# Kernel tuning notes

Measured on AMD Instinct MI355X. Metric: run time of the kernel, lower is better.

Reference implementation:

```python
import jax, jax.numpy as jnp
import numpy as np

HEADS = 16

def _binarize(W):
    # alpha: per-output-row mean of |W| (reduce over all dims except dim 0)
    alpha = jnp.mean(jnp.abs(W), axis=tuple(range(1, W.ndim)), keepdims=True)
    # straight-through sign: forward sign(W), backward identity
    B = W + jax.lax.stop_gradient(jnp.sign(W) - W)
    return alpha * B

def _binlinear(x, W, b):
    Wb = _binarize(W)
    return jnp.einsum('btc,oc->bto', x, Wb) + b

def setup_inputs() -> dict:
    key = jax.random.key(0)
    ks = jax.random.split(key, 9)
    dim = 1024
    B, T = 4, 2048
    inp = {
        'x': jax.random.normal(ks[0], (B, T, dim), jnp.float32),
        'Wq': jax.random.normal(ks[1], (dim, dim), jnp.float32) * 0.02,
        'bq': jax.random.normal(ks[2], (dim,), jnp.float32) * 0.02,
        'Wk': jax.random.normal(ks[3], (dim, dim), jnp.float32) * 0.02,
        'bk': jax.random.normal(ks[4], (dim,), jnp.float32) * 0.02,
        'Wv': jax.random.normal(ks[5], (dim, dim), jnp.float32) * 0.02,
        'bv': jax.random.normal(ks[6], (dim,), jnp.float32) * 0.02,
        'Wp': jax.random.normal(ks[7], (dim, dim), jnp.float32) * 0.02,
        'bp': jax.random.normal(ks[8], (dim,), jnp.float32) * 0.02,
    }
    return inp

def reference(x, Wq, bq, Wk, bk, Wv, bv, Wp, bp):
    B, T, C = x.shape
    H = HEADS
    Dh = C // H
    scale = Dh ** -0.5

    def split_heads(t):
        return t.reshape(B, T, H, Dh).transpose(0, 2, 1, 3)  # [B,H,T,Dh]

    q = split_heads(_binlinear(x, Wq, bq))
    k = split_heads(_binlinear(x, Wk, bk))
    v = split_heads(_binlinear(x, Wv, bv))

    att = jnp.einsum('bhtd,bhsd->bhts', q, k) * scale  # [B,H,T,T]
    att = jax.nn.softmax(att, axis=-1)
    y = jnp.einsum('bhts,bhsd->bhtd', att, v)  # [B,H,T,Dh]
    y = y.transpose(0, 2, 1, 3).reshape(B, T, C)
    return _binlinear(y, Wp, bp)
```

## Files before the change

kernel.cpp:

```cpp
#include <hip/hip_runtime.h>
#include <hip/hip_bf16.h>

typedef short s16x8 __attribute__((ext_vector_type(8)));
typedef float f32x4 __attribute__((ext_vector_type(4)));
typedef unsigned u32x4 __attribute__((ext_vector_type(4)));
typedef unsigned short u16;

#define LOG2E 1.4426950408889634f
#define QSC (0.125f * LOG2E)

typedef __attribute__((address_space(3))) unsigned int lds_u32;
typedef __attribute__((address_space(1))) const unsigned int glb_u32;

static __device__ __forceinline__ void gload16(const void* g, void* l) {
  __builtin_amdgcn_global_load_lds((glb_u32*)g, (lds_u32*)l, 16, 0, 0);
}
static __device__ __forceinline__ u16 bf16u(float f) {
  unsigned u = __builtin_bit_cast(unsigned, f);
  return (u16)((u + 0x7FFFu + ((u >> 16) & 1u)) >> 16);
}
static __device__ __forceinline__ unsigned pk(u16 a, u16 b) {
  return (unsigned)a | ((unsigned)b << 16);
}
static __device__ __forceinline__ unsigned cvtpk(float lo, float hi) {
  unsigned d;
  asm("v_cvt_pk_bf16_f32 %0, %1, %2" : "=v"(d) : "v"(lo), "v"(hi));
  return d;
}
static __device__ __forceinline__ unsigned pk2(float a, float b) {
  float2 f; f.x = a; f.y = b;
  __hip_bfloat162 h = __float22bfloat162_rn(f);
  unsigned r;
  __builtin_memcpy(&r, &h, 4);
  return r;
}

__global__ __launch_bounds__(256) void k_prep(
    const float* __restrict__ x, u16* __restrict__ xb,
    const float* __restrict__ Wq, const float* __restrict__ Wk,
    const float* __restrict__ Wv, const float* __restrict__ Wp,
    const float* __restrict__ bq, const float* __restrict__ bk,
    const float* __restrict__ bv, const float* __restrict__ bp,
    u16* __restrict__ wbqkv, u16* __restrict__ wbp,
    float* __restrict__ alphaf, float* __restrict__ biasf) {
  if (blockIdx.x >= 1024) {
    int i = ((blockIdx.x - 1024) * 256 + threadIdx.x) * 8;
    float4 a = *reinterpret_cast<const float4*>(x + i);
    float4 b = *reinterpret_cast<const float4*>(x + i + 4);
    uint4 w = { pk2(a.x, a.y), pk2(a.z, a.w), pk2(b.x, b.y), pk2(b.z, b.w) };
    *reinterpret_cast<uint4*>(xb + i) = w;
    return;
  }
  int wave = threadIdx.x >> 6, lane = threadIdx.x & 63;
  int row = blockIdx.x * 4 + wave;
  const float* src; const float* bias; int r;
  if (row < 1024)      { src = Wq; bias = bq; r = row; }
  else if (row < 2048) { src = Wk; bias = bk; r = row - 1024; }
  else if (row < 3072) { src = Wv; bias = bv; r = row - 2048; }
  else                 { src = Wp; bias = bp; r = row - 3072; }
  const float4* s4 = reinterpret_cast<const float4*>(src + r * 1024);
  float4 v[4];
  float asum = 0.f;
#pragma unroll
  for (int i = 0; i < 4; ++i) {
    v[i] = s4[lane * 4 + i];
    asum += fabsf(v[i].x) + fabsf(v[i].y) + fabsf(v[i].z) + fabsf(v[i].w);
  }
#pragma unroll
  for (int m = 32; m >= 1; m >>= 1) asum += __shfl_xor(asum, m, 64);
  float alpha = asum * (1.0f / 1024.0f);

  u16 o[16];
#pragma unroll
  for (int i = 0; i < 4; ++i) {
    const float* f = reinterpret_cast<const float*>(&v[i]);
#pragma unroll
    for (int j = 0; j < 4; ++j) {
      float w = f[j];
      o[i * 4 + j] = (w > 0.f) ? (u16)0x3F80 : ((w < 0.f) ? (u16)0xBF80 : (u16)0);
    }
  }
  u16* dst = (row < 3072 ? wbqkv + row * 1024 : wbp + (row - 3072) * 1024) + lane * 16;
  uint4 w0 = { pk(o[0],o[1]), pk(o[2],o[3]), pk(o[4],o[5]), pk(o[6],o[7]) };
  uint4 w1 = { pk(o[8],o[9]), pk(o[10],o[11]), pk(o[12],o[13]), pk(o[14],o[15]) };
  reinterpret_cast<uint4*>(dst)[0] = w0;
  reinterpret_cast<uint4*>(dst)[1] = w1;
  if (lane == 0) {
    float sc = (row < 1024) ? QSC : 1.0f;
    alphaf[row] = alpha * sc;
    biasf[row]  = bias[r] * sc;
  }
}

template <int MODE, int NX, int NWG>
__global__ __launch_bounds__(256) void k_gemm(
    const u16* __restrict__ A, const u16* __restrict__ Bw,
    const float* __restrict__ alphaf, const float* __restrict__ biasf,
    u16* __restrict__ qbuf, u16* __restrict__ kbuf, u16* __restrict__ vtbuf,
    float* __restrict__ outf) {
  __shared__ alignas(128) char smem[33792];
  char* As = smem;
  char* Bs = smem + 16384;
  int tid = threadIdx.x;
  int wave = tid >> 6, l = tid & 63, g = l >> 4, ln = l & 15;
  int wm = (wave >> 1) * 64, wn = (wave & 1) * 64;
  int wg = (blockIdx.x & 7) * (NWG / 8) + (blockIdx.x >> 3);
  int m0 = (wg / NX) * 128, n0 = (wg % NX) * 128;

  f32x4 acc[4][4];
#pragma unroll
  for (int i = 0; i < 4; ++i)
#pragma unroll
    for (int j = 0; j < 4; ++j) acc[i][j] = f32x4{0.f, 0.f, 0.f, 0.f};

  const char* Ab = reinterpret_cast<const char*>(A) + m0 * 2048;
  const char* Bb = reinterpret_cast<const char*>(Bw) + n0 * 2048;

  int soff[4];
#pragma unroll
  for (int i = 0; i < 4; ++i) {
    int P = i * 4096 + tid * 16;
    int r = P >> 7;
    int kc = ((P >> 4) & 7) ^ (r & 7);
    soff[i] = r * 2048 + kc * 16;
  }

  for (int ks = 0; ks < 16; ++ks) {
    int kb0 = ks * 128;
#pragma unroll
    for (int i = 0; i < 4; ++i)
      gload16(Ab + soff[i] + kb0, As + i * 4096 + wave * 1024);
#pragma unroll
    for (int i = 0; i < 4; ++i)
      gload16(Bb + soff[i] + kb0, Bs + i * 4096 + wave * 1024);
    __syncthreads();
#pragma unroll
    for (int kk = 0; kk < 2; ++kk) {
      s16x8 af[4], bfr[4];
#pragma unroll
      for (int mf = 0; mf < 4; ++mf) {
        int r = wm + mf * 16 + ln;
        int kb = (kk * 64 + g * 16) ^ ((r & 7) << 4);
        af[mf] = *reinterpret_cast<const s16x8*>(As + r * 128 + kb);
      }
#pragma unroll
      for (int nf = 0; nf < 4; ++nf) {
        int r = wn + nf * 16 + ln;
        int kb = (kk * 64 + g * 16) ^ ((r & 7) << 4);
        bfr[nf] = *reinterpret_cast<const s16x8*>(Bs + r * 128 + kb);
      }
#pragma unroll
      for (int mf = 0; mf < 4; ++mf)
#pragma unroll
        for (int nf = 0; nf < 4; ++nf)
          acc[mf][nf] = __builtin_amdgcn_mfma_f32_16x16x32_bf16(af[mf], bfr[nf], acc[mf][nf], 0, 0, 0);
    }
    __syncthreads();
  }

  if (MODE == 0) {
    if (n0 < 2048) {
      u16* dst = (n0 < 1024) ? qbuf : kbuf;
#pragma unroll
      for (int nf = 0; nf < 4; ++nf) {
        int n = n0 + wn + nf * 16 + ln;
        float al = alphaf[n], bi = biasf[n];
        int nl = n & 1023;
        int h = nl >> 6, d = nl & 63;
#pragma unroll
        for (int mf = 0; mf < 4; ++mf)
#pragma unroll
          for (int rg = 0; rg < 4; ++rg) {
            int m = m0 + wm + mf * 16 + g * 4 + rg;
            int b = m >> 11, t = m & 2047;
            dst[(((b * 16 + h) * 2048 + t) << 6) + d] = bf16u(al * acc[mf][nf][rg] + bi);
          }
      }
    } else {
      u16* ldsT = reinterpret_cast<u16*>(smem);
#pragma unroll
      for (int nf = 0; nf < 4; ++nf) {
        int n = n0 + wn + nf * 16 + ln;
        float al = alphaf[n], bi = biasf[n];
        int nloc = wn + nf * 16 + ln;
#pragma unroll
        for (int mf = 0; mf < 4; ++mf)
#pragma unroll
          for (int rg = 0; rg < 4; ++rg) {
            int mloc = wm + mf * 16 + g * 4 + rg;
            ldsT[mloc * 132 + nloc] = bf16u(al * acc[mf][nf][rg] + bi);
          }
      }
      __syncthreads();
      int dl = tid >> 1;
      int sh = (tid & 1) * 64;
      int nv = n0 - 2048 + dl;
      int h = nv >> 6, d = nv & 63;
      int b = m0 >> 11;
      int s0 = (m0 & 2047) + sh;
      u16* vdst = vtbuf + (((b * 16 + h) * 64 + d) << 11) + s0;
#pragma unroll
      for (int c8 = 0; c8 < 8; ++c8) {
        u16 t0 = ldsT[(sh + c8 * 8 + 0) * 132 + dl], t1 = ldsT[(sh + c8 * 8 + 1) * 132 + dl];
        u16 t2 = ldsT[(sh + c8 * 8 + 2) * 132 + dl], t3 = ldsT[(sh + c8 * 8 + 3) * 132 + dl];
        u16 t4 = ldsT[(sh + c8 * 8 + 4) * 132 + dl], t5 = ldsT[(sh + c8 * 8 + 5) * 132 + dl];
        u16 t6 = ldsT[(sh + c8 * 8 + 6) * 132 + dl], t7 = ldsT[(sh + c8 * 8 + 7) * 132 + dl];
        uint4 w = { pk(t0, t1), pk(t2, t3), pk(t4, t5), pk(t6, t7) };
        *reinterpret_cast<uint4*>(vdst + c8 * 8) = w;
      }
    }
  } else {
#pragma unroll
    for (int nf = 0; nf < 4; ++nf) {
      int n = n0 + wn + nf * 16 + ln;
      float al = alphaf[3072 + n], bi = biasf[3072 + n];
#pragma unroll
      for (int mf = 0; mf < 4; ++mf)
#pragma unroll
        for (int rg = 0; rg < 4; ++rg) {
          int m = m0 + wm + mf * 16 + g * 4 + rg;
          outf[m * 1024 + n] = al * acc[mf][nf][rg] + bi;
        }
    }
  }
}

__global__ __launch_bounds__(512, 4) void k_attn(
    const u16* __restrict__ qb, const u16* __restrict__ kb,
    const u16* __restrict__ vtb, u16* __restrict__ yb) {
  __shared__ alignas(128) char smem[32768];
  int tid = threadIdx.x;
  int wave = tid >> 6, lane = tid & 63;
  int g = lane >> 4, ln = lane & 15;

  int wg = (blockIdx.x & 7) * 64 + (blockIdx.x >> 3);
  int bh = wg >> 3, qt = wg & 7;
  const char* Qg = reinterpret_cast<const char*>(qb) + bh * 262144;
  const char* Kg = reinterpret_cast<const char*>(kb) + bh * 262144;
  const char* Vg = reinterpret_cast<const char*>(vtb) + bh * 262144;

  int qrow = qt * 256 + wave * 32 + ln;
  const s16x8* Qr0 = reinterpret_cast<const s16x8*>(Qg + qrow * 128);
  const s16x8* Qr1 = reinterpret_cast<const s16x8*>(Qg + (qrow + 16) * 128);
  s16x8 qf[2][2];
  qf[0][0] = Qr0[g]; qf[0][1] = Qr0[g + 4];
  qf[1][0] = Qr1[g]; qf[1][1] = Qr1[g + 4];

  s16x8 ones;
#pragma unroll
  for (int i = 0; i < 8; ++i) ones[i] = (short)0x3F80;

  int r = tid >> 3, kc = tid & 7;
  int wr = (r & 3) | (((r >> 3) & 1) << 2);
  int swsrc = (kc ^ wr) * 16;
  int ksrc = r * 128 + swsrc;
  int vsrc = r * 4096 + swsrc;

  int swK = (ln & 7) << 4;
  int swV = ((ln & 3) | (((ln >> 3) & 1) << 2)) << 4;

  f32x4 oacc[2][4];
#pragma unroll
  for (int s = 0; s < 2; ++s)
#pragma unroll
    for (int i = 0; i < 4; ++i) oacc[s][i] = f32x4{0.f, 0.f, 0.f, 0.f};
  f32x4 lacc[2];
  lacc[0] = f32x4{0.f, 0.f, 0.f, 0.f};
  lacc[1] = f32x4{0.f, 0.f, 0.f, 0.f};

  gload16(Kg + ksrc, smem + wave * 1024);
  gload16(Vg + vsrc, smem + 8192 + wave * 1024);
  __syncthreads();

  for (int st = 0; st < 32; ++st) {
    int cb = st & 1;
    if (st < 31) {
      int sb = (st + 1) * 64;
      char* nb = smem + (cb ^ 1) * 16384;
      gload16(Kg + sb * 128 + ksrc, nb + wave * 1024);
      gload16(Vg + sb * 2 + vsrc, nb + 8192 + wave * 1024);
    }
    const char* Kb = smem + cb * 16384;
    const char* Vb = Kb + 8192;

    f32x4 sacc[2][4];
#pragma unroll
    for (int s = 0; s < 2; ++s)
#pragma unroll
      for (int t = 0; t < 4; ++t) sacc[s][t] = f32x4{0.f, 0.f, 0.f, 0.f};
    __builtin_amdgcn_s_setprio(1);
#pragma unroll
    for (int kt = 0; kt < 2; ++kt) {
      int off = (kt * 64 + g * 16) ^ swK;
#pragma unroll
      for (int t = 0; t < 4; ++t) {
        int rho = 32 * (t & 1) + 8 * (ln >> 2) + 4 * (t >> 1) + (ln & 3);
        s16x8 kf = *reinterpret_cast<const s16x8*>(Kb + rho * 128 + off);
        sacc[0][t] = __builtin_amdgcn_mfma_f32_16x16x32_bf16(kf, qf[0][kt], sacc[0][t], 0, 0, 0);
        sacc[1][t] = __builtin_amdgcn_mfma_f32_16x16x32_bf16(kf, qf[1][kt], sacc[1][t], 0, 0, 0);
      }
    }
    __builtin_amdgcn_s_setprio(0);

    s16x8 pf[2][2];
#pragma unroll
    for (int s = 0; s < 2; ++s) {
      float p[4][4];
#pragma unroll
      for (int t = 0; t < 4; ++t)
#pragma unroll
        for (int rg = 0; rg < 4; ++rg)
          p[t][rg] = __builtin_amdgcn_exp2f(sacc[s][t][rg]);
#pragma unroll
      for (int kt = 0; kt < 2; ++kt) {
        u32x4 tw;
        tw[0] = cvtpk(p[kt][0],     p[kt][1]);
        tw[1] = cvtpk(p[kt][2],     p[kt][3]);
        tw[2] = cvtpk(p[kt + 2][0], p[kt + 2][1]);
        tw[3] = cvtpk(p[kt + 2][2], p[kt + 2][3]);
        pf[s][kt] = __builtin_bit_cast(s16x8, tw);
      }
    }

#pragma unroll
    for (int s = 0; s < 2; ++s)
#pragma unroll
      for (int kt = 0; kt < 2; ++kt)
        lacc[s] = __builtin_amdgcn_mfma_f32_16x16x32_bf16(ones, pf[s][kt], lacc[s], 0, 0, 0);

    __builtin_amdgcn_s_setprio(1);
#pragma unroll
    for (int kt = 0; kt < 2; ++kt) {
      int off = (kt * 64 + g * 16) ^ swV;
#pragma unroll
      for (int dt = 0; dt < 4; ++dt) {
        s16x8 vf = *reinterpret_cast<const s16x8*>(Vb + (dt * 16 + ln) * 128 + off);
        oacc[0][dt] = __builtin_amdgcn_mfma_f32_16x16x32_bf16(vf, pf[0][kt], oacc[0][dt], 0, 0, 0);
        oacc[1][dt] = __builtin_amdgcn_mfma_f32_16x16x32_bf16(vf, pf[1][kt], oacc[1][dt], 0, 0, 0);
      }
    }
    __builtin_amdgcn_s_setprio(0);
    __syncthreads();
  }

  int b = bh >> 4, h = bh & 15;
#pragma unroll
  for (int s = 0; s < 2; ++s) {
    float linv = 1.0f / lacc[s][0];
    u16* yrow = yb + (b * 2048 + qrow + s * 16) * 1024 + h * 64;
#pragma unroll
    for (int dt = 0; dt < 4; ++dt) {
      uint2 w;
      w.x = cvtpk(oacc[s][dt][0] * linv, oacc[s][dt][1] * linv);
      w.y = cvtpk(oacc[s][dt][2] * linv, oacc[s][dt][3] * linv);
      *reinterpret_cast<uint2*>(yrow + dt * 16 + g * 4) = w;
    }
  }
}

extern "C" void kernel_launch(void* const* d_in, const int* in_sizes, int n_in,
                              void* d_out, int out_size, void* d_ws, size_t ws_size,
                              hipStream_t stream) {
  (void)in_sizes; (void)n_in; (void)out_size; (void)ws_size;
  const float* x  = (const float*)d_in[0];
  const float* Wq = (const float*)d_in[1];
  const float* bq = (const float*)d_in[2];
  const float* Wk = (const float*)d_in[3];
  const float* bk = (const float*)d_in[4];
  const float* Wv = (const float*)d_in[5];
  const float* bv = (const float*)d_in[6];
  const float* Wp = (const float*)d_in[7];
  const float* bp = (const float*)d_in[8];

  char* ws = (char*)d_ws;
  u16*   xb    = (u16*)(ws);
  u16*   wbqkv = (u16*)(ws + 16777216);
  u16*   wbp   = (u16*)(ws + 23068672);
  float* alphaf = (float*)(ws + 25165824);
  float* biasf  = (float*)(ws + 25182208);
  u16*   vtbuf = (u16*)(ws + 25198592);
  u16*   ybuf  = xb;
  u16*   qbuf  = (u16*)d_out;
  u16*   kbuf  = (u16*)d_out + 8388608;
  float* outf  = (float*)d_out;

  k_prep<<<5120, 256, 0, stream>>>(x, xb, Wq, Wk, Wv, Wp, bq, bk, bv, bp, wbqkv, wbp, alphaf, biasf);
  k_gemm<0, 24, 1536><<<1536, 256, 0, stream>>>(xb, wbqkv, alphaf, biasf, qbuf, kbuf, vtbuf, nullptr);
  k_attn<<<512, 512, 0, stream>>>(qbuf, kbuf, vtbuf, ybuf);
  k_gemm<1, 8, 512><<<512, 256, 0, stream>>>(ybuf, wbp, alphaf, biasf, nullptr, nullptr, nullptr, outf);
}
```

Measured before the change: 165.1 us.

## Triple-buffer GEMM K-loop with async global-to-LDS prefetch two stages ahead

Replaces the single-buffered 128-wide K step in the projection GEMM with a three-stage ring of 64-wide K tiles. Loads for stage kt+2 are issued before computing stage kt, and explicit vmcnt waits plus one barrier per step replace the two syncthreads. The XOR swizzle is dropped, so the 64-byte-row LDS layout may cause bank conflicts on fragment reads, and LDS use rises to 48KB, which can lower occupancy.

```diff
diff --git a/kernel.cpp b/kernel.cpp
--- a/kernel.cpp
+++ b/kernel.cpp
@@ -98,9 +98,7 @@
     const float* __restrict__ alphaf, const float* __restrict__ biasf,
     u16* __restrict__ qbuf, u16* __restrict__ kbuf, u16* __restrict__ vtbuf,
     float* __restrict__ outf) {
-  __shared__ alignas(128) char smem[33792];
-  char* As = smem;
-  char* Bs = smem + 16384;
+  __shared__ alignas(128) char smem[49152];
   int tid = threadIdx.x;
   int wave = tid >> 6, l = tid & 63, g = l >> 4, ln = l & 15;
   int wm = (wave >> 1) * 64, wn = (wave & 1) * 64;
@@ -116,46 +114,50 @@
   const char* Ab = reinterpret_cast<const char*>(A) + m0 * 2048;
   const char* Bb = reinterpret_cast<const char*>(Bw) + n0 * 2048;
 
-  int soff[4];
-#pragma unroll
-  for (int i = 0; i < 4; ++i) {
-    int P = i * 4096 + tid * 16;
-    int r = P >> 7;
-    int kc = ((P >> 4) & 7) ^ (r & 7);
-    soff[i] = r * 2048 + kc * 16;
-  }
-
-  for (int ks = 0; ks < 16; ++ks) {
-    int kb0 = ks * 128;
-#pragma unroll
-    for (int i = 0; i < 4; ++i)
-      gload16(Ab + soff[i] + kb0, As + i * 4096 + wave * 1024);
-#pragma unroll
-    for (int i = 0; i < 4; ++i)
-      gload16(Bb + soff[i] + kb0, Bs + i * 4096 + wave * 1024);
-    __syncthreads();
-#pragma unroll
-    for (int kk = 0; kk < 2; ++kk) {
-      s16x8 af[4], bfr[4];
-#pragma unroll
-      for (int mf = 0; mf < 4; ++mf) {
-        int r = wm + mf * 16 + ln;
-        int kb = (kk * 64 + g * 16) ^ ((r & 7) << 4);
-        af[mf] = *reinterpret_cast<const s16x8*>(As + r * 128 + kb);
-      }
-#pragma unroll
-      for (int nf = 0; nf < 4; ++nf) {
-        int r = wn + nf * 16 + ln;
-        int kb = (kk * 64 + g * 16) ^ ((r & 7) << 4);
-        bfr[nf] = *reinterpret_cast<const s16x8*>(Bs + r * 128 + kb);
-      }
-#pragma unroll
-      for (int mf = 0; mf < 4; ++mf)
-#pragma unroll
-        for (int nf = 0; nf < 4; ++nf)
-          acc[mf][nf] = __builtin_amdgcn_mfma_f32_16x16x32_bf16(af[mf], bfr[nf], acc[mf][nf], 0, 0, 0);
-    }
-    __syncthreads();
+  int srow0 = tid >> 2;
+  int scol = (tid & 3) * 16;
+
+#define STAGE_G(kt)                                                          \
+  {                                                                          \
+    char* buf_ = smem + ((kt) % 3) * 16384;                                  \
+    _Pragma("unroll")                                                        \
+    for (int i_ = 0; i_ < 2; ++i_) {                                         \
+      gload16(Ab + (srow0 + 64 * i_) * 2048 + (kt) * 64 + scol,              \
+              buf_ + i_ * 4096 + wave * 1024);                               \
+      gload16(Bb + (srow0 + 64 * i_) * 2048 + (kt) * 64 + scol,              \
+              buf_ + 8192 + i_ * 4096 + wave * 1024);                        \
+    }                                                                        \
+  }
+
+  STAGE_G(0);
+  STAGE_G(1);
+  asm volatile("s_waitcnt vmcnt(4)" ::: "memory");
+  __builtin_amdgcn_sched_barrier(0);
+  __builtin_amdgcn_s_barrier();
+
+  for (int kt = 0; kt < 32; ++kt) {
+    if (kt < 30) STAGE_G(kt + 2);
+    const char* As = smem + (kt % 3) * 16384;
+    const char* Bs = As + 8192;
+    s16x8 af[4], bfr[4];
+#pragma unroll
+    for (int mf = 0; mf < 4; ++mf)
+      af[mf] = *reinterpret_cast<const s16x8*>(As + (wm + mf * 16 + ln) * 64 + g * 16);
+#pragma unroll
+    for (int nf = 0; nf < 4; ++nf)
+      bfr[nf] = *reinterpret_cast<const s16x8*>(Bs + (wn + nf * 16 + ln) * 64 + g * 16);
+#pragma unroll
+    for (int mf = 0; mf < 4; ++mf)
+#pragma unroll
+      for (int nf = 0; nf < 4; ++nf)
+        acc[mf][nf] = __builtin_amdgcn_mfma_f32_16x16x32_bf16(af[mf], bfr[nf], acc[mf][nf], 0, 0, 0);
+    if (kt < 30) {
+      asm volatile("s_waitcnt vmcnt(4)" ::: "memory");
+    } else {
+      asm volatile("s_waitcnt vmcnt(0)" ::: "memory");
+    }
+    __builtin_amdgcn_sched_barrier(0);
+    __builtin_amdgcn_s_barrier();
   }
 
   if (MODE == 0) {
@@ -223,6 +225,7 @@
         }
     }
   }
+#undef STAGE_G
 }
 
 __global__ __launch_bounds__(512, 4) void k_attn(
```

Measured after the change: 162.8 us. No clear change (-1.4%).

## Double-buffer A tiles in LDS and stream B fragments from global into registers

Applied to the files above, without the earlier changes.

Restructures the GEMM main loop into a software pipeline. The next A tile is prefetched into an alternate LDS buffer with global_load_lds while the current one feeds the MFMAs. B fragments now go straight from global memory into registers, prefetched one k-step ahead, and LDS staging for B is dropped. The loop uses one barrier per iteration with explicit vmcnt/lgkmcnt waits instead of two __syncthreads, and the kernel now requests 4 waves per SIMD through launch bounds. The goal is to hide load latency behind compute. The costs are more global traffic for B, since waves sharing a column block each fetch it, and more register pressure.

```diff
diff --git a/kernel.cpp b/kernel.cpp
--- a/kernel.cpp
+++ b/kernel.cpp
@@ -93,14 +93,12 @@
 }
 
 template <int MODE, int NX, int NWG>
-__global__ __launch_bounds__(256) void k_gemm(
+__global__ __launch_bounds__(256, 4) void k_gemm(
     const u16* __restrict__ A, const u16* __restrict__ Bw,
     const float* __restrict__ alphaf, const float* __restrict__ biasf,
     u16* __restrict__ qbuf, u16* __restrict__ kbuf, u16* __restrict__ vtbuf,
     float* __restrict__ outf) {
   __shared__ alignas(128) char smem[33792];
-  char* As = smem;
-  char* Bs = smem + 16384;
   int tid = threadIdx.x;
   int wave = tid >> 6, l = tid & 63, g = l >> 4, ln = l & 15;
   int wm = (wave >> 1) * 64, wn = (wave & 1) * 64;
@@ -124,38 +122,72 @@
     int kc = ((P >> 4) & 7) ^ (r & 7);
     soff[i] = r * 2048 + kc * 16;
   }
-
-  for (int ks = 0; ks < 16; ++ks) {
-    int kb0 = ks * 128;
-#pragma unroll
-    for (int i = 0; i < 4; ++i)
-      gload16(Ab + soff[i] + kb0, As + i * 4096 + wave * 1024);
-#pragma unroll
-    for (int i = 0; i < 4; ++i)
-      gload16(Bb + soff[i] + kb0, Bs + i * 4096 + wave * 1024);
-    __syncthreads();
-#pragma unroll
-    for (int kk = 0; kk < 2; ++kk) {
-      s16x8 af[4], bfr[4];
-#pragma unroll
-      for (int mf = 0; mf < 4; ++mf) {
-        int r = wm + mf * 16 + ln;
-        int kb = (kk * 64 + g * 16) ^ ((r & 7) << 4);
-        af[mf] = *reinterpret_cast<const s16x8*>(As + r * 128 + kb);
-      }
-#pragma unroll
-      for (int nf = 0; nf < 4; ++nf) {
-        int r = wn + nf * 16 + ln;
-        int kb = (kk * 64 + g * 16) ^ ((r & 7) << 4);
-        bfr[nf] = *reinterpret_cast<const s16x8*>(Bs + r * 128 + kb);
-      }
-#pragma unroll
-      for (int mf = 0; mf < 4; ++mf)
-#pragma unroll
-        for (int nf = 0; nf < 4; ++nf)
-          acc[mf][nf] = __builtin_amdgcn_mfma_f32_16x16x32_bf16(af[mf], bfr[nf], acc[mf][nf], 0, 0, 0);
-    }
-    __syncthreads();
+  const char* Brow[4];
+#pragma unroll
+  for (int nf = 0; nf < 4; ++nf) Brow[nf] = Bb + (wn + nf * 16 + ln) * 2048;
+
+  s16x8 bfr[2][4];
+
+#define STAGE_A(kt)                                                          \
+  {                                                                          \
+    char* buf_ = smem + ((kt) & 1) * 16384;                                  \
+    _Pragma("unroll")                                                        \
+    for (int i_ = 0; i_ < 4; ++i_)                                           \
+      gload16(Ab + soff[i_] + (kt) * 128, buf_ + i_ * 4096 + wave * 1024);   \
+  }
+#define LOAD_B(kt, kk)                                                       \
+  {                                                                          \
+    _Pragma("unroll")                                                        \
+    for (int nf_ = 0; nf_ < 4; ++nf_)                                        \
+      bfr[kk][nf_] = *reinterpret_cast<const s16x8*>(                        \
+          Brow[nf_] + (kt) * 128 + (kk) * 64 + g * 16);                      \
+  }
+
+  STAGE_A(0);
+  LOAD_B(0, 0);
+  LOAD_B(0, 1);
+  asm volatile("s_waitcnt vmcnt(8)" ::: "memory");
+  __builtin_amdgcn_sched_barrier(0);
+  __builtin_amdgcn_s_barrier();
+
+#pragma unroll
+  for (int kt = 0; kt < 16; ++kt) {
+    const char* As = smem + (kt & 1) * 16384;
+    s16x8 af[4];
+#pragma unroll
+    for (int mf = 0; mf < 4; ++mf) {
+      int r = wm + mf * 16 + ln;
+      int kb = (g * 16) ^ ((r & 7) << 4);
+      af[mf] = *reinterpret_cast<const s16x8*>(As + r * 128 + kb);
+    }
+    if (kt < 15) STAGE_A(kt + 1);
+#pragma unroll
+    for (int mf = 0; mf < 4; ++mf)
+#pragma unroll
+      for (int nf = 0; nf < 4; ++nf)
+        acc[mf][nf] = __builtin_amdgcn_mfma_f32_16x16x32_bf16(af[mf], bfr[0][nf], acc[mf][nf], 0, 0, 0);
+    if (kt < 15) LOAD_B(kt + 1, 0);
+#pragma unroll
+    for (int mf = 0; mf < 4; ++mf) {
+      int r = wm + mf * 16 + ln;
+      int kb = (64 + g * 16) ^ ((r & 7) << 4);
+      af[mf] = *reinterpret_cast<const s16x8*>(As + r * 128 + kb);
+    }
+#pragma unroll
+    for (int mf = 0; mf < 4; ++mf)
+#pragma unroll
+      for (int nf = 0; nf < 4; ++nf)
+        acc[mf][nf] = __builtin_amdgcn_mfma_f32_16x16x32_bf16(af[mf], bfr[1][nf], acc[mf][nf], 0, 0, 0);
+    if (kt < 15) LOAD_B(kt + 1, 1);
+
+    asm volatile("s_waitcnt lgkmcnt(0)" ::: "memory");
+    if (kt < 15) {
+      asm volatile("s_waitcnt vmcnt(8)" ::: "memory");
+    } else {
+      asm volatile("s_waitcnt vmcnt(0)" ::: "memory");
+    }
+    __builtin_amdgcn_sched_barrier(0);
+    __builtin_amdgcn_s_barrier();
   }
 
   if (MODE == 0) {
@@ -223,6 +255,8 @@
         }
     }
   }
+#undef STAGE_A
+#undef LOAD_B
 }
 
 __global__ __launch_bounds__(512, 4) void k_attn(
```

After: 219.8 us (median of 2 runs). +33.1%, slower.
